# Kernel optimization log

Hardware: AMD Instinct MI355X
Metric: run time of the kernel (lower is better)

The kernel has to match this reference:

```python
import jax, jax.numpy as jnp
import numpy as np

NUM_MOVIES = 100000
MOVIE_FEAT = 128
USER_FEAT = 128
BATCH = 16384
N_NBRS = 50
D0, D1, D2 = 256, 256, 128  # layer_dims


def setup_inputs() -> dict:
    key = jax.random.key(0)
    ks = jax.random.split(key, 16)
    inp = {
        "users": jax.random.normal(ks[0], (BATCH, USER_FEAT), jnp.float32),
        "pos_movies": jax.random.normal(ks[1], (BATCH, MOVIE_FEAT), jnp.float32),
        "neg_movies": jax.random.normal(ks[2], (BATCH, MOVIE_FEAT), jnp.float32),
        "user_ids": jax.random.randint(ks[3], (BATCH,), 0, BATCH),
        "pos_movie_ids": jax.random.randint(ks[4], (BATCH,), 0, NUM_MOVIES),
        "neg_movie_ids": jax.random.randint(ks[5], (BATCH,), 0, NUM_MOVIES),
        "nbr_ids": jax.random.randint(ks[6], (BATCH, N_NBRS), 0, NUM_MOVIES),
        # learned params / buffers
        "movie_table": jax.random.normal(ks[7], (NUM_MOVIES, MOVIE_FEAT), jnp.float32),
        "Wu": jax.random.normal(ks[8], (USER_FEAT, D0), jnp.float32) * (1.0 / np.sqrt(USER_FEAT)),
        "bu": jnp.zeros((D0,), jnp.float32),
        "Wm": jax.random.normal(ks[9], (MOVIE_FEAT, D0), jnp.float32) * (1.0 / np.sqrt(MOVIE_FEAT)),
        "bm": jnp.zeros((D0,), jnp.float32),
        "W1": jax.random.normal(ks[10], (D0, D1), jnp.float32) * (1.0 / np.sqrt(D0)),
        "b1": jnp.zeros((D1,), jnp.float32),
        "W2": jax.random.normal(ks[11], (D1, D2), jnp.float32) * (1.0 / np.sqrt(D1)),
        "b2": jnp.zeros((D2,), jnp.float32),
    }
    return inp


def reference(users, pos_movies, neg_movies, user_ids, pos_movie_ids, neg_movie_ids,
              nbr_ids, movie_table, Wu, bu, Wm, bm, W1, b1, W2, b2):
    # user_projection / movie_projection
    user_emb = users @ Wu + bu                      # [B, D0]
    movie_emb = movie_table @ Wm + bm               # [N, D0]
    pos_emb = movie_emb[pos_movie_ids]              # [B, D0]
    neg_emb = movie_emb[neg_movie_ids]              # [B, D0]
    # vectorized replacement of the per-user neighbor gather + mean loop
    nbr_mean = jnp.mean(movie_emb[nbr_ids], axis=1)  # [B, N_NBRS, D0] -> [B, D0]
    user_emb = user_emb + nbr_mean
    x = jnp.stack([user_emb, pos_emb, neg_emb], axis=0)  # [3, B, D0]
    x = jax.nn.relu(x @ W1 + b1)
    x = jax.nn.relu(x @ W2 + b2)
    return (x[0], x[1], x[2])
```

## Files before the change

kernel.cpp:

```cpp
#include <hip/hip_runtime.h>
#include <hip/hip_bf16.h>

#define BATCH_N   16384
#define FEAT      128
#define NNBR      50
#define NUM_MOVIES_N 100000

typedef short  short8  __attribute__((ext_vector_type(8)));
typedef float  floatx4 __attribute__((ext_vector_type(4)));
typedef unsigned int u32;

__device__ __forceinline__ __hip_bfloat16 f2bf(float x) { return __float2bfloat16(x); }
__device__ __forceinline__ float bfb2f(short s) {
  union { u32 u; float f; } c; c.u = ((u32)(unsigned short)s) << 16; return c.f;
}

__device__ __forceinline__ void gld16(const __hip_bfloat16* g, __hip_bfloat16* l) {
  __builtin_amdgcn_global_load_lds(
      (const __attribute__((address_space(1))) u32*)g,
      (__attribute__((address_space(3))) u32*)l, 16, 0, 0);
}

__device__ __forceinline__ floatx4 mfma16(short8 a, short8 b, floatx4 c) {
  return __builtin_amdgcn_mfma_f32_16x16x32_bf16(a, b, c, 0, 0, 0);
}

__global__ __launch_bounds__(256) void conv_table(
    const float* __restrict__ t, __hip_bfloat16* __restrict__ tb) {
  size_t i = ((size_t)blockIdx.x * 256 + threadIdx.x) * 8;
  float4 v0 = *(const float4*)(t + i);
  float4 v1 = *(const float4*)(t + i + 4);
  __hip_bfloat16 o[8];
  o[0] = f2bf(v0.x); o[1] = f2bf(v0.y); o[2] = f2bf(v0.z); o[3] = f2bf(v0.w);
  o[4] = f2bf(v1.x); o[5] = f2bf(v1.y); o[6] = f2bf(v1.z); o[7] = f2bf(v1.w);
  *(short8*)(tb + i) = *(short8*)o;
}

__global__ __launch_bounds__(256) void prep_kernel(
    const float* __restrict__ Wu, const float* __restrict__ Wm,
    const float* __restrict__ W1, const float* __restrict__ W2,
    const float* __restrict__ bu, const float* __restrict__ bm,
    __hip_bfloat16* __restrict__ WcatT, __hip_bfloat16* __restrict__ WmT,
    __hip_bfloat16* __restrict__ W1T,  __hip_bfloat16* __restrict__ W2T,
    float* __restrict__ bc) {
  int idx = blockIdx.x * 256 + threadIdx.x;
  int n = idx & 255, k = idx >> 8;
  float v = (k < 128) ? Wu[k * 256 + n] : Wm[(k - 128) * 256 + n];
  WcatT[n * 256 + k] = f2bf(v);
  W1T[n * 256 + k]   = f2bf(W1[k * 256 + n]);
  if (k < 128) WmT[n * 128 + k] = f2bf(Wm[k * 256 + n]);
  if (idx < 32768) {
    int k2 = idx >> 7, n2 = idx & 127;
    W2T[n2 * 256 + k2] = f2bf(W2[k2 * 128 + n2]);
  }
  if (idx < 256) bc[idx] = bu[idx] + bm[idx];
}

__global__ __launch_bounds__(256) void gather_user(
    const float* __restrict__ users, const int* __restrict__ nbr_ids,
    const __hip_bfloat16* __restrict__ tb, __hip_bfloat16* __restrict__ A_user) {
  int row  = (blockIdx.x << 2) + (threadIdx.x >> 6);
  int lane = threadIdx.x & 63;
  int quad = lane >> 4, sl = lane & 15;
  const int* nb = nbr_ids + row * NNBR;
  float acc[8] = {0.f, 0.f, 0.f, 0.f, 0.f, 0.f, 0.f, 0.f};
  #pragma unroll
  for (int it = 0; it < 13; ++it) {
    int j = it * 4 + quad;
    if (j < NNBR) {
      int id = nb[j];
      short8 v = *(const short8*)(tb + (size_t)id * FEAT + sl * 8);
      #pragma unroll
      for (int e = 0; e < 8; ++e) acc[e] += bfb2f(v[e]);
    }
  }
  __hip_bfloat16 o[8];
  #pragma unroll
  for (int e = 0; e < 8; ++e) {
    float v = acc[e];
    v += __shfl_xor(v, 16, 64);
    v += __shfl_xor(v, 32, 64);
    o[e] = f2bf(v * (1.f / NNBR));
  }
  if (quad == 0)
    *(short8*)(A_user + (size_t)row * 256 + 128 + sl * 8) = *(short8*)o;
  float2 uv = ((const float2*)(users + (size_t)row * FEAT))[lane];
  __hip_bfloat162 t0; t0.x = f2bf(uv.x); t0.y = f2bf(uv.y);
  ((__hip_bfloat162*)(A_user + (size_t)row * 256))[lane] = t0;
}

template <int K0, int NCOL, bool RELU, bool TOGLB>
__device__ __forceinline__ void run_layer(
    const __hip_bfloat16* Ain, __hip_bfloat16* Bst,
    const __hip_bfloat16* __restrict__ W, const float* __restrict__ bias,
    __hip_bfloat16* Olds, float* __restrict__ Oglb,
    int t, int wm, int wn, int quad, int lrow, long m0) {
  constexpr int KK = K0 / 32;
  constexpr int JN = NCOL / 32;
  floatx4 acc[2][JN] = {};
  for (int kc = 0; kc < KK; ++kc) {
    const int k0 = kc * 32;
    __syncthreads();
    #pragma unroll
    for (int i = 0; i < NCOL / 64; ++i) {
      int c = t + i * 256;
      int n = c >> 2, q = c & 3;
      gld16(W + (size_t)n * K0 + k0 + ((q ^ ((n >> 1) & 3)) << 3),
            Bst + (c << 3));
    }
    __syncthreads();
    short8 af[2];
    #pragma unroll
    for (int i = 0; i < 2; ++i) {
      int r = wm * 32 + i * 16 + lrow;
      af[i] = *(const short8*)&Ain[r * K0 + ((((k0 >> 3) + quad) ^ (r & 7)) << 3)];
    }
    #pragma unroll
    for (int j = 0; j < JN; ++j) {
      int n = wn * (NCOL / 2) + j * 16 + lrow;
      short8 bf = *(const short8*)&Bst[n * 32 + ((quad ^ ((n >> 1) & 3)) << 3)];
      acc[0][j] = mfma16(af[0], bf, acc[0][j]);
      acc[1][j] = mfma16(af[1], bf, acc[1][j]);
    }
  }
  __syncthreads();
  #pragma unroll
  for (int j = 0; j < JN; ++j) {
    int col = wn * (NCOL / 2) + j * 16 + lrow;
    float bv = bias[col];
    #pragma unroll
    for (int i = 0; i < 2; ++i)
      #pragma unroll
      for (int r = 0; r < 4; ++r) {
        int row = wm * 32 + i * 16 + quad * 4 + r;
        float v = acc[i][j][r] + bv;
        if (RELU) v = fmaxf(v, 0.f);
        if (TOGLB) {
          Oglb[(m0 + row) * 128 + col] = v;
        } else {
          int ch = col >> 3;
          Olds[row * 256 + (((ch ^ (row & 7)) << 3) | (col & 7))] = f2bf(v);
        }
      }
  }
}

__global__ __launch_bounds__(256, 2) void fused_mlp(
    const __hip_bfloat16* __restrict__ A_user,
    const __hip_bfloat16* __restrict__ tb,
    const int* __restrict__ pos_ids, const int* __restrict__ neg_ids,
    const __hip_bfloat16* __restrict__ WcatT,
    const __hip_bfloat16* __restrict__ WmT,
    const __hip_bfloat16* __restrict__ W1T,
    const __hip_bfloat16* __restrict__ W2T,
    const float* __restrict__ bc, const float* __restrict__ bmv,
    const float* __restrict__ b1, const float* __restrict__ b2,
    float* __restrict__ out) {
  __shared__ __hip_bfloat16 A_lds[64 * 256];
  __shared__ __hip_bfloat16 E_lds[64 * 256];

  const int t    = threadIdx.x;
  const int lane = t & 63, wid = t >> 6;
  const int wm   = wid & 1, wn = wid >> 1;
  const int quad = lane >> 4, lrow = lane & 15;
  const int bx   = blockIdx.x;
  const int s    = bx % 3;
  const long m0  = (long)(bx / 3) * 64;

  if (s == 0) {
    #pragma unroll
    for (int i = 0; i < 8; ++i) {
      int c = t + i * 256;
      int r = c >> 5, kq = c & 31;
      gld16(A_user + ((size_t)(m0 + r) << 8) + ((kq ^ (r & 7)) << 3),
            A_lds + (c << 3));
    }
  } else {
    const int* ids = (s == 1) ? pos_ids : neg_ids;
    #pragma unroll
    for (int i = 0; i < 4; ++i) {
      int c = t + i * 256;
      int r = c >> 4, kq = c & 15;
      int id = ids[m0 + r];
      gld16(tb + ((size_t)id << 7) + ((kq ^ (r & 7)) << 3),
            A_lds + (c << 3));
    }
  }

  if (s == 0)
    run_layer<256, 256, false, false>(A_lds, E_lds, WcatT, bc, E_lds, nullptr,
                                      t, wm, wn, quad, lrow, m0);
  else
    run_layer<128, 256, false, false>(A_lds, E_lds, WmT, bmv, E_lds, nullptr,
                                      t, wm, wn, quad, lrow, m0);

  run_layer<256, 256, true, false>(E_lds, A_lds, W1T, b1, A_lds, nullptr,
                                   t, wm, wn, quad, lrow, m0);

  run_layer<256, 128, true, true>(A_lds, E_lds, W2T, b2, nullptr,
                                  out + (size_t)s * BATCH_N * 128,
                                  t, wm, wn, quad, lrow, m0);
}

extern "C" void kernel_launch(void* const* d_in, const int* in_sizes, int n_in,
                              void* d_out, int out_size, void* d_ws, size_t ws_size,
                              hipStream_t stream) {
  const float* users   = (const float*)d_in[0];
  const int*   pos_ids = (const int*)d_in[4];
  const int*   neg_ids = (const int*)d_in[5];
  const int*   nbr_ids = (const int*)d_in[6];
  const float* table   = (const float*)d_in[7];
  const float* Wu = (const float*)d_in[8];
  const float* bu = (const float*)d_in[9];
  const float* Wm = (const float*)d_in[10];
  const float* bm = (const float*)d_in[11];
  const float* W1 = (const float*)d_in[12];
  const float* b1 = (const float*)d_in[13];
  const float* W2 = (const float*)d_in[14];
  const float* b2 = (const float*)d_in[15];
  float* out = (float*)d_out;

  char* p = (char*)d_ws;
  auto carve = [&](size_t bytes) { char* r = p; p += (bytes + 255) & ~(size_t)255; return r; };
  __hip_bfloat16* tb     = (__hip_bfloat16*)carve((size_t)NUM_MOVIES_N * FEAT * 2);
  __hip_bfloat16* WcatT  = (__hip_bfloat16*)carve(256 * 256 * 2);
  __hip_bfloat16* WmT    = (__hip_bfloat16*)carve(256 * 128 * 2);
  __hip_bfloat16* W1T    = (__hip_bfloat16*)carve(256 * 256 * 2);
  __hip_bfloat16* W2T    = (__hip_bfloat16*)carve(128 * 256 * 2);
  float*          bc     = (float*)carve(256 * 4);
  __hip_bfloat16* A_user = (__hip_bfloat16*)carve((size_t)BATCH_N * 256 * 2);

  conv_table<<<NUM_MOVIES_N * FEAT / (256 * 8), 256, 0, stream>>>(table, tb);
  prep_kernel<<<256, 256, 0, stream>>>(Wu, Wm, W1, W2, bu, bm,
                                       WcatT, WmT, W1T, W2T, bc);
  gather_user<<<BATCH_N / 4, 256, 0, stream>>>(users, nbr_ids, tb, A_user);
  fused_mlp<<<dim3(3 * BATCH_N / 64), 256, 0, stream>>>(
      A_user, tb, pos_ids, neg_ids, WcatT, WmT, W1T, W2T,
      bc, bm, b1, b2, out);
}
```

Baseline: 214.9 us.

## Hold weight fragments in registers, widen MLP blocks to 512 threads, merge prep kernels

Result: faster. 204.2 us (-5.0%).

```diff
diff --git a/kernel.cpp b/kernel.cpp
--- a/kernel.cpp
+++ b/kernel.cpp
@@ -25,35 +25,37 @@
   return __builtin_amdgcn_mfma_f32_16x16x32_bf16(a, b, c, 0, 0, 0);
 }
 
-__global__ __launch_bounds__(256) void conv_table(
-    const float* __restrict__ t, __hip_bfloat16* __restrict__ tb) {
-  size_t i = ((size_t)blockIdx.x * 256 + threadIdx.x) * 8;
-  float4 v0 = *(const float4*)(t + i);
-  float4 v1 = *(const float4*)(t + i + 4);
-  __hip_bfloat16 o[8];
-  o[0] = f2bf(v0.x); o[1] = f2bf(v0.y); o[2] = f2bf(v0.z); o[3] = f2bf(v0.w);
-  o[4] = f2bf(v1.x); o[5] = f2bf(v1.y); o[6] = f2bf(v1.z); o[7] = f2bf(v1.w);
-  *(short8*)(tb + i) = *(short8*)o;
-}
-
-__global__ __launch_bounds__(256) void prep_kernel(
+#define CONV_BLOCKS (NUM_MOVIES_N * FEAT / (256 * 8))
+__global__ __launch_bounds__(256) void prep_all(
+    const float* __restrict__ t, __hip_bfloat16* __restrict__ tb,
     const float* __restrict__ Wu, const float* __restrict__ Wm,
     const float* __restrict__ W1, const float* __restrict__ W2,
     const float* __restrict__ bu, const float* __restrict__ bm,
     __hip_bfloat16* __restrict__ WcatT, __hip_bfloat16* __restrict__ WmT,
     __hip_bfloat16* __restrict__ W1T,  __hip_bfloat16* __restrict__ W2T,
     float* __restrict__ bc) {
-  int idx = blockIdx.x * 256 + threadIdx.x;
-  int n = idx & 255, k = idx >> 8;
-  float v = (k < 128) ? Wu[k * 256 + n] : Wm[(k - 128) * 256 + n];
-  WcatT[n * 256 + k] = f2bf(v);
-  W1T[n * 256 + k]   = f2bf(W1[k * 256 + n]);
-  if (k < 128) WmT[n * 128 + k] = f2bf(Wm[k * 256 + n]);
-  if (idx < 32768) {
-    int k2 = idx >> 7, n2 = idx & 127;
-    W2T[n2 * 256 + k2] = f2bf(W2[k2 * 128 + n2]);
-  }
-  if (idx < 256) bc[idx] = bu[idx] + bm[idx];
+  int bid = blockIdx.x;
+  if (bid < CONV_BLOCKS) {
+    size_t i = ((size_t)bid * 256 + threadIdx.x) * 8;
+    float4 v0 = *(const float4*)(t + i);
+    float4 v1 = *(const float4*)(t + i + 4);
+    __hip_bfloat16 o[8];
+    o[0] = f2bf(v0.x); o[1] = f2bf(v0.y); o[2] = f2bf(v0.z); o[3] = f2bf(v0.w);
+    o[4] = f2bf(v1.x); o[5] = f2bf(v1.y); o[6] = f2bf(v1.z); o[7] = f2bf(v1.w);
+    *(short8*)(tb + i) = *(short8*)o;
+  } else {
+    int idx = (bid - CONV_BLOCKS) * 256 + threadIdx.x;
+    int n = idx & 255, k = idx >> 8;
+    float v = (k < 128) ? Wu[k * 256 + n] : Wm[(k - 128) * 256 + n];
+    WcatT[n * 256 + k] = f2bf(v);
+    W1T[n * 256 + k]   = f2bf(W1[k * 256 + n]);
+    if (k < 128) WmT[n * 128 + k] = f2bf(Wm[k * 256 + n]);
+    if (idx < 32768) {
+      int k2 = idx >> 7, n2 = idx & 127;
+      W2T[n2 * 256 + k2] = f2bf(W2[k2 * 128 + n2]);
+    }
+    if (idx < 256) bc[idx] = bu[idx] + bm[idx];
+  }
 }
 
 __global__ __launch_bounds__(256) void gather_user(
@@ -90,62 +92,64 @@
 }
 
 template <int K0, int NCOL, bool RELU, bool TOGLB>
-__device__ __forceinline__ void run_layer(
-    const __hip_bfloat16* Ain, __hip_bfloat16* Bst,
-    const __hip_bfloat16* __restrict__ W, const float* __restrict__ bias,
+__device__ __forceinline__ void layer(
+    const __hip_bfloat16* Ain,
+    const __hip_bfloat16* __restrict__ Wt, const float* __restrict__ bias,
     __hip_bfloat16* Olds, float* __restrict__ Oglb,
-    int t, int wm, int wn, int quad, int lrow, long m0) {
+    int wid, int quad, int lrow) {
   constexpr int KK = K0 / 32;
-  constexpr int JN = NCOL / 32;
-  floatx4 acc[2][JN] = {};
-  for (int kc = 0; kc < KK; ++kc) {
-    const int k0 = kc * 32;
-    __syncthreads();
-    #pragma unroll
-    for (int i = 0; i < NCOL / 64; ++i) {
-      int c = t + i * 256;
-      int n = c >> 2, q = c & 3;
-      gld16(W + (size_t)n * K0 + k0 + ((q ^ ((n >> 1) & 3)) << 3),
-            Bst + (c << 3));
-    }
-    __syncthreads();
-    short8 af[2];
-    #pragma unroll
-    for (int i = 0; i < 2; ++i) {
-      int r = wm * 32 + i * 16 + lrow;
-      af[i] = *(const short8*)&Ain[r * K0 + ((((k0 >> 3) + quad) ^ (r & 7)) << 3)];
-    }
+  constexpr int JN = NCOL / 128;
+  const int c0 = wid * JN * 16;
+
+  short8 bfr[JN][KK];
+  float  bv[JN];
+  #pragma unroll
+  for (int j = 0; j < JN; ++j) {
+    #pragma unroll
+    for (int kc = 0; kc < KK; ++kc)
+      bfr[j][kc] = *(const short8*)(Wt + (size_t)(c0 + j * 16 + lrow) * K0 +
+                                    kc * 32 + quad * 8);
+    bv[j] = bias[c0 + j * 16 + lrow];
+  }
+
+  #pragma unroll
+  for (int it = 0; it < 4; ++it) {
+    int r = it * 16 + lrow;
+    short8 af[KK];
+    #pragma unroll
+    for (int kc = 0; kc < KK; ++kc)
+      af[kc] = *(const short8*)&Ain[r * K0 + (((kc * 4 + quad) ^ (r & 7)) << 3)];
+    floatx4 pa[JN], pb[JN];
+    #pragma unroll
+    for (int j = 0; j < JN; ++j) { pa[j] = {}; pb[j] = {}; }
+    #pragma unroll
+    for (int kc = 0; kc < KK; kc += 2)
+      #pragma unroll
+      for (int j = 0; j < JN; ++j) {
+        pa[j] = mfma16(af[kc],     bfr[j][kc],     pa[j]);
+        pb[j] = mfma16(af[kc + 1], bfr[j][kc + 1], pb[j]);
+      }
     #pragma unroll
     for (int j = 0; j < JN; ++j) {
-      int n = wn * (NCOL / 2) + j * 16 + lrow;
-      short8 bf = *(const short8*)&Bst[n * 32 + ((quad ^ ((n >> 1) & 3)) << 3)];
-      acc[0][j] = mfma16(af[0], bf, acc[0][j]);
-      acc[1][j] = mfma16(af[1], bf, acc[1][j]);
-    }
-  }
-  __syncthreads();
-  #pragma unroll
-  for (int j = 0; j < JN; ++j) {
-    int col = wn * (NCOL / 2) + j * 16 + lrow;
-    float bv = bias[col];
-    #pragma unroll
-    for (int i = 0; i < 2; ++i)
+      floatx4 a = pa[j] + pb[j];
+      int col = c0 + j * 16 + lrow;
       #pragma unroll
-      for (int r = 0; r < 4; ++r) {
-        int row = wm * 32 + i * 16 + quad * 4 + r;
-        float v = acc[i][j][r] + bv;
+      for (int rr = 0; rr < 4; ++rr) {
+        int row = it * 16 + quad * 4 + rr;
+        float v = a[rr] + bv[j];
         if (RELU) v = fmaxf(v, 0.f);
         if (TOGLB) {
-          Oglb[(m0 + row) * 128 + col] = v;
+          Oglb[(size_t)row * NCOL + col] = v;
         } else {
           int ch = col >> 3;
           Olds[row * 256 + (((ch ^ (row & 7)) << 3) | (col & 7))] = f2bf(v);
         }
       }
-  }
-}
-
-__global__ __launch_bounds__(256, 2) void fused_mlp(
+    }
+  }
+}
+
+__global__ __launch_bounds__(512, 2) void fused_mlp(
     const __hip_bfloat16* __restrict__ A_user,
     const __hip_bfloat16* __restrict__ tb,
     const int* __restrict__ pos_ids, const int* __restrict__ neg_ids,
@@ -161,45 +165,46 @@
 
   const int t    = threadIdx.x;
   const int lane = t & 63, wid = t >> 6;
-  const int wm   = wid & 1, wn = wid >> 1;
   const int quad = lane >> 4, lrow = lane & 15;
-  const int bx   = blockIdx.x;
-  const int s    = bx % 3;
-  const long m0  = (long)(bx / 3) * 64;
+  const int s    = blockIdx.x % 3;
+  const long m0  = (long)(blockIdx.x / 3) * 64;
 
   if (s == 0) {
     #pragma unroll
-    for (int i = 0; i < 8; ++i) {
-      int c = t + i * 256;
-      int r = c >> 5, kq = c & 31;
-      gld16(A_user + ((size_t)(m0 + r) << 8) + ((kq ^ (r & 7)) << 3),
+    for (int i = 0; i < 4; ++i) {
+      int c = t + i * 512;
+      int r = c >> 5, sl = c & 31;
+      gld16(A_user + ((size_t)(m0 + r) << 8) + ((sl ^ (r & 7)) << 3),
             A_lds + (c << 3));
     }
   } else {
     const int* ids = (s == 1) ? pos_ids : neg_ids;
     #pragma unroll
-    for (int i = 0; i < 4; ++i) {
-      int c = t + i * 256;
-      int r = c >> 4, kq = c & 15;
+    for (int i = 0; i < 2; ++i) {
+      int c = t + i * 512;
+      int r = c >> 4, sl = c & 15;
       int id = ids[m0 + r];
-      gld16(tb + ((size_t)id << 7) + ((kq ^ (r & 7)) << 3),
+      gld16(tb + ((size_t)id << 7) + ((sl ^ (r & 7)) << 3),
             A_lds + (c << 3));
     }
   }
+  __syncthreads();
 
   if (s == 0)
-    run_layer<256, 256, false, false>(A_lds, E_lds, WcatT, bc, E_lds, nullptr,
-                                      t, wm, wn, quad, lrow, m0);
+    layer<256, 256, false, false>(A_lds, WcatT, bc, E_lds, nullptr,
+                                  wid, quad, lrow);
   else
-    run_layer<128, 256, false, false>(A_lds, E_lds, WmT, bmv, E_lds, nullptr,
-                                      t, wm, wn, quad, lrow, m0);
-
-  run_layer<256, 256, true, false>(E_lds, A_lds, W1T, b1, A_lds, nullptr,
-                                   t, wm, wn, quad, lrow, m0);
-
-  run_layer<256, 128, true, true>(A_lds, E_lds, W2T, b2, nullptr,
-                                  out + (size_t)s * BATCH_N * 128,
-                                  t, wm, wn, quad, lrow, m0);
+    layer<128, 256, false, false>(A_lds, WmT, bmv, E_lds, nullptr,
+                                  wid, quad, lrow);
+  __syncthreads();
+
+  layer<256, 256, true, false>(E_lds, W1T, b1, A_lds, nullptr,
+                               wid, quad, lrow);
+  __syncthreads();
+
+  layer<256, 128, true, true>(A_lds, W2T, b2, nullptr,
+                              out + ((size_t)s * BATCH_N + m0) * 128,
+                              wid, quad, lrow);
 }
 
 extern "C" void kernel_launch(void* const* d_in, const int* in_sizes, int n_in,
@@ -230,11 +235,10 @@
   float*          bc     = (float*)carve(256 * 4);
   __hip_bfloat16* A_user = (__hip_bfloat16*)carve((size_t)BATCH_N * 256 * 2);
 
-  conv_table<<<NUM_MOVIES_N * FEAT / (256 * 8), 256, 0, stream>>>(table, tb);
-  prep_kernel<<<256, 256, 0, stream>>>(Wu, Wm, W1, W2, bu, bm,
-                                       WcatT, WmT, W1T, W2T, bc);
+  prep_all<<<CONV_BLOCKS + 256, 256, 0, stream>>>(
+      table, tb, Wu, Wm, W1, W2, bu, bm, WcatT, WmT, W1T, W2T, bc);
   gather_user<<<BATCH_N / 4, 256, 0, stream>>>(users, nbr_ids, tb, A_user);
-  fused_mlp<<<dim3(3 * BATCH_N / 64), 256, 0, stream>>>(
+  fused_mlp<<<3 * BATCH_N / 64, 512, 0, stream>>>(
       A_user, tb, pos_ids, neg_ids, WcatT, WmT, W1T, W2T,
       bc, bm, b1, b2, out);
 }
```
